# Kernel tuning notes

Hardware: AMD Instinct MI355X
Metric: run time of the kernel (lower is better)

Reference implementation:

```python
import jax, jax.numpy as jnp
import numpy as np

N_NODES = 100000
N_EDGES = 300000
D = 128
HID = 128

def setup_inputs() -> dict:
    key = jax.random.key(0)
    ks = jax.random.split(key, 12)
    s = lambda fan_in: 1.0 / np.sqrt(fan_in)
    return {
        "user_emb": jax.random.normal(ks[0], (N_NODES, D), jnp.float32),
        "item_emb": jax.random.normal(ks[1], (N_NODES, D), jnp.float32),
        "ei_ui": jax.random.randint(ks[2], (2, N_EDGES), 0, N_NODES, jnp.int64),
        "ei_iu": jax.random.randint(ks[3], (2, N_EDGES), 0, N_NODES, jnp.int64),
        "W_bi_ui": jax.random.normal(ks[4], (2 * D, HID), jnp.float32) * s(2 * D),
        "b_bi_ui": jnp.zeros((HID,), jnp.float32),
        "W1_ui": jax.random.normal(ks[5], (HID, HID), jnp.float32) * s(HID),
        "b1_ui": jnp.zeros((HID,), jnp.float32),
        "W2_ui": jax.random.normal(ks[6], (HID, 1), jnp.float32) * s(HID),
        "b2_ui": jnp.zeros((1,), jnp.float32),
        "W_bi_iu": jax.random.normal(ks[7], (2 * D, HID), jnp.float32) * s(2 * D),
        "b_bi_iu": jnp.zeros((HID,), jnp.float32),
        "W1_iu": jax.random.normal(ks[8], (HID, HID), jnp.float32) * s(HID),
        "b1_iu": jnp.zeros((HID,), jnp.float32),
        "W2_iu": jax.random.normal(ks[9], (HID, 1), jnp.float32) * s(HID),
        "b2_iu": jnp.zeros((1,), jnp.float32),
    }

def _decode_edge_type(src_emb, dst_emb, edge_index, W_bi, b_bi, W1, b1, W2, b2):
    # gather endpoint embeddings and concat -> [E, 2D]
    e = jnp.concatenate([src_emb[edge_index[0]], dst_emb[edge_index[1]]], axis=1)
    h = jax.nn.elu(e @ W_bi + b_bi)          # bilinear -> ELU
    h = jax.nn.elu(h @ W1 + b1)              # linear1 -> ELU
    p = jax.nn.sigmoid(h @ W2 + b2)          # linear2 -> sigmoid
    return p.reshape(-1)                     # [E]

def reference(user_emb, item_emb, ei_ui, ei_iu,
              W_bi_ui, b_bi_ui, W1_ui, b1_ui, W2_ui, b2_ui,
              W_bi_iu, b_bi_iu, W1_iu, b1_iu, W2_iu, b2_iu):
    # edge type (user, clicks, item): source=user, target=item
    p_ui = _decode_edge_type(user_emb, item_emb, ei_ui,
                             W_bi_ui, b_bi_ui, W1_ui, b1_ui, W2_ui, b2_ui)
    # edge type (item, clicked_by, user): source=item, target=user
    p_iu = _decode_edge_type(item_emb, user_emb, ei_iu,
                             W_bi_iu, b_bi_iu, W1_iu, b1_iu, W2_iu, b2_iu)
    return jnp.stack([p_ui, p_iu])  # [2, E]
```

## Files before the change

kernel.cpp:

```cpp
#include <hip/hip_runtime.h>

typedef __attribute__((ext_vector_type(8))) short short8;
typedef __attribute__((ext_vector_type(4))) float float4v;
typedef __attribute__((ext_vector_type(4))) int int4v;
typedef __attribute__((ext_vector_type(2))) int int2v;

#define E_EDGES 300000
#define EPB 256
#define NBLK ((E_EDGES + EPB - 1) / EPB)
#define TAB_ELEMS 12800000

__device__ __forceinline__ short f2bf(float f) {
    unsigned u = __float_as_uint(f);
    return (short)((u + 0x7FFFu + ((u >> 16) & 1u)) >> 16);
}
__device__ __forceinline__ unsigned pk_bf16(float a, float b) {
    unsigned ua = __float_as_uint(a), ub = __float_as_uint(b);
    ua += 0x7FFFu + ((ua >> 16) & 1u);
    ub += 0x7FFFu + ((ub >> 16) & 1u);
    return __builtin_amdgcn_perm(ub, ua, 0x07060302);
}
__device__ __forceinline__ unsigned cvtpk(float a, float b) {
    unsigned r;
    __asm__("v_cvt_pk_bf16_f32 %0, %1, %2" : "=v"(r) : "v"(a), "v"(b));
    return r;
}
__device__ __forceinline__ void cp16(const void* g, void* l) {
    __builtin_amdgcn_global_load_lds(
        (const __attribute__((address_space(1))) unsigned int*)g,
        (__attribute__((address_space(3))) unsigned int*)l, 16, 0, 0);
}

__global__ void prep_all(const float* __restrict__ ue, const float* __restrict__ ie,
                         const float* __restrict__ Wbi_ui, const float* __restrict__ W1_ui,
                         const float* __restrict__ Wbi_iu, const float* __restrict__ W1_iu,
                         short* __restrict__ ws) {
    __shared__ short tr[64 * 68];
    const int t = blockIdx.y;
    const int tid = threadIdx.x;
    if (blockIdx.x < 1024) {
        const float* src = t ? ie : ue;
        short* dst = ws + 98304 + (size_t)t * TAB_ELEMS;
        const int stride = 1024 * 256;
        for (int g = blockIdx.x * 256 + tid; g < TAB_ELEMS / 8; g += stride) {
            const float* p = src + (size_t)g * 8;
            float4v v0 = ((const float4v*)p)[0];
            float4v v1 = ((const float4v*)p)[1];
            int4v w = { (int)pk_bf16(v0[0], v0[1]), (int)pk_bf16(v0[2], v0[3]),
                        (int)pk_bf16(v1[0], v1[1]), (int)pk_bf16(v1[2], v1[3]) };
            *(int4v*)(dst + (size_t)g * 8) = w;
        }
        return;
    }
    const int m = blockIdx.x - 1024;
    const float* W; int k0, n0, obase;
    if (m < 8) {
        int kt = m >> 1, nh = m & 1;
        W = t ? Wbi_iu : Wbi_ui; k0 = kt * 64; n0 = nh * 64;
        obase = t * 32768 + kt * 8192;
    } else {
        int mm = m - 8; int kt = mm >> 1, nh = mm & 1;
        W = t ? W1_iu : W1_ui; k0 = kt * 64; n0 = nh * 64;
        obase = 65536 + t * 16384 + kt * 8192;
    }
    for (int it = 0; it < 16; ++it) {
        int flat = it * 256 + tid;
        int kk = flat >> 6, nn = flat & 63;
        tr[nn * 68 + kk] = f2bf(W[(size_t)(k0 + kk) * 128 + n0 + nn]);
    }
    __syncthreads();
    for (int it = 0; it < 16; ++it) {
        int flat = it * 256 + tid;
        int nn = flat >> 6, kk = flat & 63;
        int n = n0 + nn;
        ws[obase + n * 64 + (kk ^ ((n & 7) << 3))] = tr[nn * 68 + kk];
    }
}

template<bool BF16G>
__launch_bounds__(512, 4)
__global__ void edge_decoder(
    const float* __restrict__ user_emb, const float* __restrict__ item_emb,
    const int* __restrict__ ei_ui, const int* __restrict__ ei_iu,
    const float* __restrict__ b_bi_ui, const float* __restrict__ b1_ui,
    const float* __restrict__ W2_ui, const float* __restrict__ b2_ui,
    const float* __restrict__ b_bi_iu, const float* __restrict__ b1_iu,
    const float* __restrict__ W2_iu, const float* __restrict__ b2_iu,
    const short* __restrict__ ws, const short* __restrict__ tab,
    float* __restrict__ out)
{
    __shared__ short Blds[2][128 * 64];
    __shared__ short HL[8 * 2048];

    const int type = blockIdx.y;
    const int tid = threadIdx.x;
    const int wave = tid >> 6, lane = tid & 63;
    const int q = lane >> 4, ln = lane & 15;
    const int e0 = blockIdx.x * EPB;

    const int*   ei   = type ? ei_iu : ei_ui;
    const float* bbi  = type ? b_bi_iu : b_bi_ui;
    const float* b1v  = type ? b1_iu : b1_ui;
    const float* W2v  = type ? W2_iu : W2_ui;
    const float* b2v  = type ? b2_iu : b2_ui;
    const short* WbiT = ws + type * 32768;
    const short* W1T  = ws + 65536 + type * 16384;

    #pragma unroll
    for (int c = 0; c < 2; ++c)
        cp16(WbiT + c * 4096 + tid * 8, &Blds[0][c * 4096 + tid * 8]);

    int si[2], di[2];
    #pragma unroll
    for (int mt = 0; mt < 2; ++mt) {
        int erow = e0 + wave * 32 + mt * 16 + ln;
        int safe = (erow < E_EDGES) ? erow : 0;
        si[mt] = ei[safe];
        di[mt] = ei[E_EDGES + safe];
    }

    const short* sp[2]; const short* dp[2];
    const float* spf[2]; const float* dpf[2];
    if (BF16G) {
        #pragma unroll
        for (int mt = 0; mt < 2; ++mt) {
            sp[mt] = tab + (size_t)(type ? TAB_ELEMS : 0) + (size_t)si[mt] * 128 + q * 8;
            dp[mt] = tab + (size_t)(type ? 0 : TAB_ELEMS) + (size_t)di[mt] * 128 + q * 8;
        }
    } else {
        const float* srcT = type ? item_emb : user_emb;
        const float* dstT = type ? user_emb : item_emb;
        #pragma unroll
        for (int mt = 0; mt < 2; ++mt) {
            spf[mt] = srcT + (size_t)si[mt] * 128 + q * 8;
            dpf[mt] = dstT + (size_t)di[mt] * 128 + q * 8;
        }
    }

    short8 aA[2][2], aB[2][2];

#define GATHER(BUF, HALF, OFF) do { \
    _Pragma("unroll") \
    for (int mt = 0; mt < 2; ++mt) { \
        _Pragma("unroll") \
        for (int k2 = 0; k2 < 2; ++k2) { \
            if (BF16G) { \
                BUF[mt][k2] = *(const short8*)((HALF ? dp[mt] : sp[mt]) + OFF + k2 * 32); \
            } else { \
                const float* p = (HALF ? dpf[mt] : spf[mt]) + OFF + k2 * 32; \
                float4v v0 = ((const float4v*)p)[0]; \
                float4v v1 = ((const float4v*)p)[1]; \
                int4v w = { (int)pk_bf16(v0[0], v0[1]), (int)pk_bf16(v0[2], v0[3]), \
                            (int)pk_bf16(v1[0], v1[1]), (int)pk_bf16(v1[2], v1[3]) }; \
                BUF[mt][k2] = *(short8*)&w; \
            } \
        } \
    } } while (0)

    GATHER(aA, 0, 0);
    GATHER(aB, 0, 64);

    float4v acc[2][8];
    #pragma unroll
    for (int nt = 0; nt < 8; ++nt) {
        acc[0][nt] = *(const float4v*)(bbi + nt * 16 + q * 4);
        acc[1][nt] = acc[0][nt];
    }

    const int swz = (ln & 7) << 3;
    const int hswz = ((ln & 7) << 1) | (ln & 8);

#define L1_TILE(KT, ABUF) do { \
    __syncthreads(); \
    const short* nxt = (KT < 3) ? (WbiT + (KT + 1) * 8192) : W1T; \
    _Pragma("unroll") \
    for (int c = 0; c < 2; ++c) \
        cp16(nxt + c * 4096 + tid * 8, &Blds[(KT + 1) & 1][c * 4096 + tid * 8]); \
    __builtin_amdgcn_s_setprio(1); \
    _Pragma("unroll") \
    for (int ks2 = 0; ks2 < 2; ++ks2) { \
        int ka = (ks2 * 32 + q * 8) ^ swz; \
        _Pragma("unroll") \
        for (int nt = 0; nt < 8; ++nt) { \
            short8 bf = *(const short8*)&Blds[KT & 1][(nt * 16 + ln) * 64 + ka]; \
            acc[0][nt] = __builtin_amdgcn_mfma_f32_16x16x32_bf16(bf, ABUF[0][ks2], acc[0][nt], 0, 0, 0); \
            acc[1][nt] = __builtin_amdgcn_mfma_f32_16x16x32_bf16(bf, ABUF[1][ks2], acc[1][nt], 0, 0, 0); \
        } \
    } \
    __builtin_amdgcn_s_setprio(0); \
    } while (0)

    L1_TILE(0, aA);
    GATHER(aA, 1, 0);
    L1_TILE(1, aB);
    GATHER(aB, 1, 64);
    L1_TILE(2, aA);
    L1_TILE(3, aB);

    __syncthreads();

    #pragma unroll
    for (int c = 0; c < 2; ++c)
        cp16(W1T + 8192 + c * 4096 + tid * 8, &Blds[1][c * 4096 + tid * 8]);

    short* Hw = &HL[wave * 2048];
    short8 a2[2][4];
    #pragma unroll
    for (int mt = 0; mt < 2; ++mt) {
        #pragma unroll
        for (int nt = 0; nt < 8; ++nt) {
            float4v v = acc[mt][nt];
            float x0 = v[0] > 0.f ? v[0] : (__expf(v[0]) - 1.f);
            float x1 = v[1] > 0.f ? v[1] : (__expf(v[1]) - 1.f);
            float x2 = v[2] > 0.f ? v[2] : (__expf(v[2]) - 1.f);
            float x3 = v[3] > 0.f ? v[3] : (__expf(v[3]) - 1.f);
            int g = (4 * nt + q) ^ hswz;
            *(int2v*)(Hw + ln * 128 + g * 4) =
                (int2v){ (int)cvtpk(x0, x1), (int)cvtpk(x2, x3) };
        }
        #pragma unroll
        for (int ks = 0; ks < 4; ++ks) {
            int g = (8 * ks + 2 * q) ^ hswz;
            a2[mt][ks] = *(const short8*)(Hw + ln * 128 + g * 4);
        }
    }

    #pragma unroll
    for (int nt = 0; nt < 8; ++nt) {
        acc[0][nt] = *(const float4v*)(b1v + nt * 16 + q * 4);
        acc[1][nt] = acc[0][nt];
    }

#define L2_TILE(KT) do { \
    if (KT == 1) __syncthreads(); \
    __builtin_amdgcn_s_setprio(1); \
    _Pragma("unroll") \
    for (int ks2 = 0; ks2 < 2; ++ks2) { \
        int ka = (ks2 * 32 + q * 8) ^ swz; \
        _Pragma("unroll") \
        for (int nt = 0; nt < 8; ++nt) { \
            short8 bf = *(const short8*)&Blds[KT][(nt * 16 + ln) * 64 + ka]; \
            acc[0][nt] = __builtin_amdgcn_mfma_f32_16x16x32_bf16(bf, a2[0][KT * 2 + ks2], acc[0][nt], 0, 0, 0); \
            acc[1][nt] = __builtin_amdgcn_mfma_f32_16x16x32_bf16(bf, a2[1][KT * 2 + ks2], acc[1][nt], 0, 0, 0); \
        } \
    } \
    __builtin_amdgcn_s_setprio(0); \
    } while (0)

    L2_TILE(0);
    L2_TILE(1);

    float4v w2q[8];
    #pragma unroll
    for (int nt = 0; nt < 8; ++nt)
        w2q[nt] = *(const float4v*)(W2v + nt * 16 + q * 4);
    const float b2s = b2v[0];

    #pragma unroll
    for (int mt = 0; mt < 2; ++mt) {
        float s = 0.f;
        #pragma unroll
        for (int nt = 0; nt < 8; ++nt) {
            float4v v = acc[mt][nt];
            float4v w = w2q[nt];
            float x;
            x = v[0]; x = x > 0.f ? x : (__expf(x) - 1.f); s += x * w[0];
            x = v[1]; x = x > 0.f ? x : (__expf(x) - 1.f); s += x * w[1];
            x = v[2]; x = x > 0.f ? x : (__expf(x) - 1.f); s += x * w[2];
            x = v[3]; x = x > 0.f ? x : (__expf(x) - 1.f); s += x * w[3];
        }
        s += __shfl_xor(s, 16);
        s += __shfl_xor(s, 32);
        if (q == mt) {
            int e = e0 + wave * 32 + mt * 16 + ln;
            if (e < E_EDGES) {
                float z = s + b2s;
                out[type * E_EDGES + e] = 1.f / (1.f + __expf(-z));
            }
        }
    }
#undef GATHER
#undef L1_TILE
#undef L2_TILE
}

extern "C" void kernel_launch(void* const* d_in, const int* in_sizes, int n_in,
                              void* d_out, int out_size, void* d_ws, size_t ws_size,
                              hipStream_t stream) {
    const float* user_emb = (const float*)d_in[0];
    const float* item_emb = (const float*)d_in[1];
    const int*   ei_ui    = (const int*)d_in[2];
    const int*   ei_iu    = (const int*)d_in[3];
    const float* W_bi_ui  = (const float*)d_in[4];
    const float* b_bi_ui  = (const float*)d_in[5];
    const float* W1_ui    = (const float*)d_in[6];
    const float* b1_ui    = (const float*)d_in[7];
    const float* W2_ui    = (const float*)d_in[8];
    const float* b2_ui    = (const float*)d_in[9];
    const float* W_bi_iu  = (const float*)d_in[10];
    const float* b_bi_iu  = (const float*)d_in[11];
    const float* W1_iu    = (const float*)d_in[12];
    const float* b1_iu    = (const float*)d_in[13];
    const float* W2_iu    = (const float*)d_in[14];
    const float* b2_iu    = (const float*)d_in[15];
    short* ws  = (short*)d_ws;
    short* tab = ws + 98304;
    float* out = (float*)d_out;

    const size_t need = 98304u * 2u + (size_t)2 * TAB_ELEMS * 2u;

    hipLaunchKernelGGL(prep_all, dim3(1036, 2), dim3(256), 0, stream,
                       user_emb, item_emb, W_bi_ui, W1_ui, W_bi_iu, W1_iu, ws);
    if (ws_size >= need) {
        edge_decoder<true><<<dim3(NBLK, 2), dim3(512), 0, stream>>>(
            user_emb, item_emb, ei_ui, ei_iu,
            b_bi_ui, b1_ui, W2_ui, b2_ui,
            b_bi_iu, b1_iu, W2_iu, b2_iu,
            ws, tab, out);
    } else {
        edge_decoder<false><<<dim3(NBLK, 2), dim3(512), 0, stream>>>(
            user_emb, item_emb, ei_ui, ei_iu,
            b_bi_ui, b1_ui, W2_ui, b2_ui,
            b_bi_iu, b1_iu, W2_iu, b2_iu,
            ws, tab, out);
    }
}
```

Baseline: 236.7 us.

## Gather fp32 embeddings directly and drop full-table bf16 conversion prepass

Removes the prepass kernel that converted both full embedding tables to bf16 on every call. The decoder now gathers fp32 rows and converts them in registers with the packed bf16 convert instruction. This removes a large streaming read and write of the whole tables, at the cost of doubling bytes per gathered row. The H staging buffer in LDS also switches from an XOR swizzle to row padding.

```diff
diff --git a/kernel.cpp b/kernel.cpp
--- a/kernel.cpp
+++ b/kernel.cpp
@@ -8,17 +8,10 @@
 #define E_EDGES 300000
 #define EPB 256
 #define NBLK ((E_EDGES + EPB - 1) / EPB)
-#define TAB_ELEMS 12800000
 
 __device__ __forceinline__ short f2bf(float f) {
     unsigned u = __float_as_uint(f);
     return (short)((u + 0x7FFFu + ((u >> 16) & 1u)) >> 16);
-}
-__device__ __forceinline__ unsigned pk_bf16(float a, float b) {
-    unsigned ua = __float_as_uint(a), ub = __float_as_uint(b);
-    ua += 0x7FFFu + ((ua >> 16) & 1u);
-    ub += 0x7FFFu + ((ub >> 16) & 1u);
-    return __builtin_amdgcn_perm(ub, ua, 0x07060302);
 }
 __device__ __forceinline__ unsigned cvtpk(float a, float b) {
     unsigned r;
@@ -31,28 +24,13 @@
         (__attribute__((address_space(3))) unsigned int*)l, 16, 0, 0);
 }
 
-__global__ void prep_all(const float* __restrict__ ue, const float* __restrict__ ie,
-                         const float* __restrict__ Wbi_ui, const float* __restrict__ W1_ui,
-                         const float* __restrict__ Wbi_iu, const float* __restrict__ W1_iu,
-                         short* __restrict__ ws) {
+__global__ void prep_w(const float* __restrict__ Wbi_ui, const float* __restrict__ W1_ui,
+                       const float* __restrict__ Wbi_iu, const float* __restrict__ W1_iu,
+                       short* __restrict__ ws) {
     __shared__ short tr[64 * 68];
     const int t = blockIdx.y;
     const int tid = threadIdx.x;
-    if (blockIdx.x < 1024) {
-        const float* src = t ? ie : ue;
-        short* dst = ws + 98304 + (size_t)t * TAB_ELEMS;
-        const int stride = 1024 * 256;
-        for (int g = blockIdx.x * 256 + tid; g < TAB_ELEMS / 8; g += stride) {
-            const float* p = src + (size_t)g * 8;
-            float4v v0 = ((const float4v*)p)[0];
-            float4v v1 = ((const float4v*)p)[1];
-            int4v w = { (int)pk_bf16(v0[0], v0[1]), (int)pk_bf16(v0[2], v0[3]),
-                        (int)pk_bf16(v1[0], v1[1]), (int)pk_bf16(v1[2], v1[3]) };
-            *(int4v*)(dst + (size_t)g * 8) = w;
-        }
-        return;
-    }
-    const int m = blockIdx.x - 1024;
+    const int m = blockIdx.x;
     const float* W; int k0, n0, obase;
     if (m < 8) {
         int kt = m >> 1, nh = m & 1;
@@ -77,7 +55,6 @@
     }
 }
 
-template<bool BF16G>
 __launch_bounds__(512, 4)
 __global__ void edge_decoder(
     const float* __restrict__ user_emb, const float* __restrict__ item_emb,
@@ -86,11 +63,10 @@
     const float* __restrict__ W2_ui, const float* __restrict__ b2_ui,
     const float* __restrict__ b_bi_iu, const float* __restrict__ b1_iu,
     const float* __restrict__ W2_iu, const float* __restrict__ b2_iu,
-    const short* __restrict__ ws, const short* __restrict__ tab,
-    float* __restrict__ out)
+    const short* __restrict__ ws, float* __restrict__ out)
 {
     __shared__ short Blds[2][128 * 64];
-    __shared__ short HL[8 * 2048];
+    __shared__ short HL[8 * 2176];
 
     const int type = blockIdx.y;
     const int tid = threadIdx.x;
@@ -105,6 +81,8 @@
     const float* b2v  = type ? b2_iu : b2_ui;
     const short* WbiT = ws + type * 32768;
     const short* W1T  = ws + 65536 + type * 16384;
+    const float* srcT = type ? item_emb : user_emb;
+    const float* dstT = type ? user_emb : item_emb;
 
     #pragma unroll
     for (int c = 0; c < 2; ++c)
@@ -119,22 +97,11 @@
         di[mt] = ei[E_EDGES + safe];
     }
 
-    const short* sp[2]; const short* dp[2];
     const float* spf[2]; const float* dpf[2];
-    if (BF16G) {
-        #pragma unroll
-        for (int mt = 0; mt < 2; ++mt) {
-            sp[mt] = tab + (size_t)(type ? TAB_ELEMS : 0) + (size_t)si[mt] * 128 + q * 8;
-            dp[mt] = tab + (size_t)(type ? 0 : TAB_ELEMS) + (size_t)di[mt] * 128 + q * 8;
-        }
-    } else {
-        const float* srcT = type ? item_emb : user_emb;
-        const float* dstT = type ? user_emb : item_emb;
-        #pragma unroll
-        for (int mt = 0; mt < 2; ++mt) {
-            spf[mt] = srcT + (size_t)si[mt] * 128 + q * 8;
-            dpf[mt] = dstT + (size_t)di[mt] * 128 + q * 8;
-        }
+    #pragma unroll
+    for (int mt = 0; mt < 2; ++mt) {
+        spf[mt] = srcT + (size_t)si[mt] * 128 + q * 8;
+        dpf[mt] = dstT + (size_t)di[mt] * 128 + q * 8;
     }
 
     short8 aA[2][2], aB[2][2];
@@ -144,16 +111,12 @@
     for (int mt = 0; mt < 2; ++mt) { \
         _Pragma("unroll") \
         for (int k2 = 0; k2 < 2; ++k2) { \
-            if (BF16G) { \
-                BUF[mt][k2] = *(const short8*)((HALF ? dp[mt] : sp[mt]) + OFF + k2 * 32); \
-            } else { \
-                const float* p = (HALF ? dpf[mt] : spf[mt]) + OFF + k2 * 32; \
-                float4v v0 = ((const float4v*)p)[0]; \
-                float4v v1 = ((const float4v*)p)[1]; \
-                int4v w = { (int)pk_bf16(v0[0], v0[1]), (int)pk_bf16(v0[2], v0[3]), \
-                            (int)pk_bf16(v1[0], v1[1]), (int)pk_bf16(v1[2], v1[3]) }; \
-                BUF[mt][k2] = *(short8*)&w; \
-            } \
+            const float* p = (HALF ? dpf[mt] : spf[mt]) + OFF + k2 * 32; \
+            float4v v0 = ((const float4v*)p)[0]; \
+            float4v v1 = ((const float4v*)p)[1]; \
+            int4v w = { (int)cvtpk(v0[0], v0[1]), (int)cvtpk(v0[2], v0[3]), \
+                        (int)cvtpk(v1[0], v1[1]), (int)cvtpk(v1[2], v1[3]) }; \
+            BUF[mt][k2] = *(short8*)&w; \
         } \
     } } while (0)
 
@@ -168,7 +131,6 @@
     }
 
     const int swz = (ln & 7) << 3;
-    const int hswz = ((ln & 7) << 1) | (ln & 8);
 
 #define L1_TILE(KT, ABUF) do { \
     __syncthreads(); \
@@ -203,7 +165,7 @@
     for (int c = 0; c < 2; ++c)
         cp16(W1T + 8192 + c * 4096 + tid * 8, &Blds[1][c * 4096 + tid * 8]);
 
-    short* Hw = &HL[wave * 2048];
+    short* Hw = &HL[wave * 2176];
     short8 a2[2][4];
     #pragma unroll
     for (int mt = 0; mt < 2; ++mt) {
@@ -214,15 +176,12 @@
             float x1 = v[1] > 0.f ? v[1] : (__expf(v[1]) - 1.f);
             float x2 = v[2] > 0.f ? v[2] : (__expf(v[2]) - 1.f);
             float x3 = v[3] > 0.f ? v[3] : (__expf(v[3]) - 1.f);
-            int g = (4 * nt + q) ^ hswz;
-            *(int2v*)(Hw + ln * 128 + g * 4) =
+            *(int2v*)(Hw + ln * 136 + (4 * nt + q) * 4) =
                 (int2v){ (int)cvtpk(x0, x1), (int)cvtpk(x2, x3) };
         }
         #pragma unroll
-        for (int ks = 0; ks < 4; ++ks) {
-            int g = (8 * ks + 2 * q) ^ hswz;
-            a2[mt][ks] = *(const short8*)(Hw + ln * 128 + g * 4);
-        }
+        for (int ks = 0; ks < 4; ++ks)
+            a2[mt][ks] = *(const short8*)(Hw + ln * 136 + (8 * ks + 2 * q) * 4);
     }
 
     #pragma unroll
@@ -304,24 +263,13 @@
     const float* W2_iu    = (const float*)d_in[14];
     const float* b2_iu    = (const float*)d_in[15];
     short* ws  = (short*)d_ws;
-    short* tab = ws + 98304;
     float* out = (float*)d_out;
 
-    const size_t need = 98304u * 2u + (size_t)2 * TAB_ELEMS * 2u;
-
-    hipLaunchKernelGGL(prep_all, dim3(1036, 2), dim3(256), 0, stream,
-                       user_emb, item_emb, W_bi_ui, W1_ui, W_bi_iu, W1_iu, ws);
-    if (ws_size >= need) {
-        edge_decoder<true><<<dim3(NBLK, 2), dim3(512), 0, stream>>>(
-            user_emb, item_emb, ei_ui, ei_iu,
-            b_bi_ui, b1_ui, W2_ui, b2_ui,
-            b_bi_iu, b1_iu, W2_iu, b2_iu,
-            ws, tab, out);
-    } else {
-        edge_decoder<false><<<dim3(NBLK, 2), dim3(512), 0, stream>>>(
-            user_emb, item_emb, ei_ui, ei_iu,
-            b_bi_ui, b1_ui, W2_ui, b2_ui,
-            b_bi_iu, b1_iu, W2_iu, b2_iu,
-            ws, tab, out);
-    }
-}
+    hipLaunchKernelGGL(prep_w, dim3(12, 2), dim3(256), 0, stream,
+                       W_bi_ui, W1_ui, W_bi_iu, W1_iu, ws);
+    edge_decoder<<<dim3(NBLK, 2), dim3(512), 0, stream>>>(
+        user_emb, item_emb, ei_ui, ei_iu,
+        b_bi_ui, b1_ui, W2_ui, b2_ui,
+        b_bi_iu, b1_iu, W2_iu, b2_iu,
+        ws, out);
+}
```

Measured after the change: 267.7 us. +13.1%, slower.
